# Optimization experiments

Hardware: AMD Instinct MI355X
Metric: run time of the kernel (lower is better)

Reference implementation:

```python
import jax, jax.numpy as jnp
import numpy as np

N = 50000   # nodes
E = 800000  # edges (avg degree 16)
R = 3       # relations (distance bins)
IN = 3      # node_input_dim
H = 64      # hidden_dim
EA = 6      # edge_input_dim
DH = 32     # decoder_hidden_dim


def setup_inputs() -> dict:
    key = jax.random.key(0)
    ks = jax.random.split(key, 16)
    x = jax.random.normal(ks[0], (N, IN), jnp.float32)
    edge_index = jax.random.randint(ks[1], (2, E), 0, N)
    edge_attr = jax.random.uniform(ks[2], (E, EA), dtype=jnp.float32)
    # scale log1p-distance column so edges span all 3 bins (thresholds ~8.52, ~9.21)
    edge_attr = edge_attr.at[:, 0].mul(12.0)
    p = lambda k, s: jax.random.normal(k, s, jnp.float32) * 0.1
    return dict(
        x=x, edge_index=edge_index, edge_attr=edge_attr,
        w0=p(ks[3], (R, IN, H)), root0=p(ks[4], (IN, H)), b0=jnp.zeros((H,), jnp.float32),
        w1=p(ks[5], (R, H, H)),  root1=p(ks[6], (H, H)),  b1=jnp.zeros((H,), jnp.float32),
        w2=p(ks[7], (R, H, H)),  root2=p(ks[8], (H, H)),  b2=jnp.zeros((H,), jnp.float32),
        ln_g0=jnp.ones((H,), jnp.float32), ln_b0=jnp.zeros((H,), jnp.float32),
        ln_g1=jnp.ones((H,), jnp.float32), ln_b1=jnp.zeros((H,), jnp.float32),
        ln_g2=jnp.ones((H,), jnp.float32), ln_b2=jnp.zeros((H,), jnp.float32),
        res_w=p(ks[9], (IN, H)), res_b=jnp.zeros((H,), jnp.float32),
        dec_w1=p(ks[10], (4 * H + EA, DH)), dec_b1=jnp.zeros((DH,), jnp.float32),
        dec_w2=p(ks[11], (DH, DH // 2)),    dec_b2=jnp.zeros((DH // 2,), jnp.float32),
        dec_w3=p(ks[12], (DH // 2, 1)),     dec_b3=jnp.zeros((1,), jnp.float32),
    )


def _layernorm(v, g, b, eps=1e-5):
    mu = v.mean(-1, keepdims=True)
    var = ((v - mu) ** 2).mean(-1, keepdims=True)
    return (v - mu) / jnp.sqrt(var + eps) * g + b


def reference(x, edge_index, edge_attr,
              w0, root0, b0, w1, root1, b1, w2, root2, b2,
              ln_g0, ln_b0, ln_g1, ln_b1, ln_g2, ln_b2,
              res_w, res_b,
              dec_w1, dec_b1, dec_w2, dec_b2, dec_w3, dec_b3):
    dist = edge_attr[:, 0]
    q1 = jnp.log1p(jnp.float32(5000.0))
    q2 = jnp.log1p(jnp.float32(10000.0))
    edge_type = (dist > q1).astype(jnp.int32) + (dist > q2).astype(jnp.int32)  # [E]
    src, dst = edge_index[0], edge_index[1]

    def rgcn(xi, W, root, b):
        # RGCNConv with per-relation mean aggregation:
        # out_i = root x_i + b + sum_r W_r * mean_{j in N_r(i)} x_j
        # aggregate-then-transform: segment-sum masked source feats, divide by
        # per-relation in-degree, then one small [in,H] matmul per relation.
        xs = xi[src]                                  # [E, in] gather
        out = xi @ root + b                           # [N, H]
        for r in range(R):
            m = (edge_type == r).astype(xi.dtype)[:, None]
            s = jax.ops.segment_sum(xs * m, dst, num_segments=N)   # [N, in]
            c = jax.ops.segment_sum(m, dst, num_segments=N)        # [N, 1]
            out = out + (s / jnp.maximum(c, 1.0)) @ W[r]
        return out

    # encoder (eval mode -> dropout is identity)
    h = jax.nn.relu(rgcn(x, w0, root0, b0))
    h1 = _layernorm(h + x @ res_w + res_b, ln_g0, ln_b0)
    h = jax.nn.relu(rgcn(h1, w1, root1, b1))
    h2 = _layernorm(h + h1, ln_g1, ln_b1)
    h = jax.nn.relu(rgcn(h2, w2, root2, b2))
    h3 = _layernorm(h + h2, ln_g2, ln_b2)

    # edge decoder
    hs, hd = h3[src], h3[dst]                         # [E, H] gathers
    dec_in = jnp.concatenate([hs, hd, jnp.abs(hs - hd), hs * hd, edge_attr], axis=-1)
    z = jax.nn.relu(dec_in @ dec_w1 + dec_b1)
    z = jax.nn.relu(z @ dec_w2 + dec_b2)
    return (z @ dec_w3 + dec_b3).squeeze(-1)          # [E]
```

## Files before the change

kernel.cpp:

```cpp
#include <hip/hip_runtime.h>
#include <math.h>

#define NN 50000
#define NE 800000
#define HD 64
#define NB 196
#define DT 5

typedef float f32x4 __attribute__((ext_vector_type(4)));
typedef float f32x16 __attribute__((ext_vector_type(16)));
typedef short short8 __attribute__((ext_vector_type(8)));
typedef _Float16 hf2 __attribute__((ext_vector_type(2)));
typedef _Float16 half8 __attribute__((ext_vector_type(8)));

__device__ __forceinline__ float wave_sum(float v) {
  #pragma unroll
  for (int off = 32; off > 0; off >>= 1) v += __shfl_xor(v, off, 64);
  return v;
}

__device__ __forceinline__ unsigned f2h_pk(float a, float b) {
  auto v = __builtin_amdgcn_cvt_pkrtz(a, b);
  union { decltype(v) h; unsigned u; } cv; cv.h = v; return cv.u;
}
__device__ __forceinline__ unsigned short f2h(float a) {
  union { _Float16 h; unsigned short u; } cv; cv.h = (_Float16)a; return cv.u;
}
__device__ __forceinline__ float h2f(unsigned short b) {
  union { unsigned short u; _Float16 h; } v; v.u = b; return (float)v.h;
}

__global__ __launch_bounds__(256) void edge_prep(
    const int* __restrict__ ei, const float* __restrict__ ea,
    int* __restrict__ cntR, unsigned char* __restrict__ r8)
{
  int e = blockIdx.x * blockDim.x + threadIdx.x;
  if (e >= NE) return;
  float dist = ea[e * 6];
  const float q1 = log1pf(5000.0f);
  const float q2 = log1pf(10000.0f);
  int r = (dist > q1 ? 1 : 0) + (dist > q2 ? 1 : 0);
  r8[e] = (unsigned char)r;
  int d = ei[NE + e];
  atomicAdd(&cntR[d * 3 + r], 1);
}

__global__ __launch_bounds__(256) void scanA(const int* __restrict__ cntR, int* __restrict__ bsum) {
  __shared__ int sd[256];
  int n = blockIdx.x * 256 + threadIdx.x;
  int deg = 0;
  if (n < NN) deg = cntR[3 * n] + cntR[3 * n + 1] + cntR[3 * n + 2];
  sd[threadIdx.x] = deg;
  __syncthreads();
  #pragma unroll
  for (int s = 128; s > 0; s >>= 1) {
    if (threadIdx.x < s) sd[threadIdx.x] += sd[threadIdx.x + s];
    __syncthreads();
  }
  if (threadIdx.x == 0) bsum[blockIdx.x] = sd[0];
}

__global__ __launch_bounds__(256) void scanB(int* __restrict__ bsum) {
  __shared__ int sd[256];
  int v = (threadIdx.x < NB) ? bsum[threadIdx.x] : 0;
  sd[threadIdx.x] = v;
  __syncthreads();
  for (int s = 1; s < 256; s <<= 1) {
    int t = (threadIdx.x >= s) ? sd[threadIdx.x - s] : 0;
    __syncthreads();
    sd[threadIdx.x] += t;
    __syncthreads();
  }
  if (threadIdx.x < NB) bsum[threadIdx.x] = sd[threadIdx.x] - v;
}

__global__ __launch_bounds__(256) void scanC(
    const int* __restrict__ cntR, const int* __restrict__ bsum,
    int* __restrict__ off3, int* __restrict__ cursor3, float* __restrict__ dinv)
{
  __shared__ int sd[256];
  int n = blockIdx.x * 256 + threadIdx.x;
  int c0 = 0, c1 = 0, c2 = 0;
  if (n < NN) { c0 = cntR[3 * n]; c1 = cntR[3 * n + 1]; c2 = cntR[3 * n + 2]; }
  int deg = c0 + c1 + c2;
  sd[threadIdx.x] = deg;
  __syncthreads();
  for (int s = 1; s < 256; s <<= 1) {
    int t = (threadIdx.x >= s) ? sd[threadIdx.x - s] : 0;
    __syncthreads();
    sd[threadIdx.x] += t;
    __syncthreads();
  }
  if (n < NN) {
    int o = bsum[blockIdx.x] + sd[threadIdx.x] - deg;
    off3[3 * n + 0] = o;           cursor3[3 * n + 0] = o;
    off3[3 * n + 1] = o + c0;      cursor3[3 * n + 1] = o + c0;
    off3[3 * n + 2] = o + c0 + c1; cursor3[3 * n + 2] = o + c0 + c1;
    dinv[3 * n + 0] = 1.0f / (float)(c0 > 1 ? c0 : 1);
    dinv[3 * n + 1] = 1.0f / (float)(c1 > 1 ? c1 : 1);
    dinv[3 * n + 2] = 1.0f / (float)(c2 > 1 ? c2 : 1);
  }
}

__global__ __launch_bounds__(256) void scatter_kernel(
    const int* __restrict__ ei, const unsigned char* __restrict__ r8,
    int* __restrict__ cursor3, unsigned short* __restrict__ sorted)
{
  int e = blockIdx.x * blockDim.x + threadIdx.x;
  if (e >= NE) return;
  int r = r8[e];
  int s = ei[e], d = ei[NE + e];
  int pos = atomicAdd(&cursor3[d * 3 + r], 1);
  sorted[pos] = (unsigned short)s;
}

__global__ __launch_bounds__(256) void agg0_pack(
    const float* __restrict__ x, const int* __restrict__ off3, const int* __restrict__ cntR,
    const unsigned short* __restrict__ sorted, float* __restrict__ agg0,
    const float* __restrict__ W1, const float* __restrict__ W2,
    const float* __restrict__ root1, const float* __restrict__ w1,
    const float* __restrict__ root2, const float* __restrict__ w2,
    unsigned short* __restrict__ pk3, unsigned short* __restrict__ pk2,
    unsigned short* __restrict__ pkl1, unsigned short* __restrict__ pkl2)
{
  if (blockIdx.x < 3) {
    if (blockIdx.x == 0) {
      for (int idx = threadIdx.x; idx < 8704; idx += 256) {
        int j = idx & 7, l = (idx >> 3) & 63, t = idx >> 9;
        int k = 16 * t + 8 * (l >> 5) + j;
        int n = l & 31;
        pk3[idx] = (k < 262) ? f2h(W1[k * 32 + n]) : (unsigned short)0;
      }
      for (int idx = threadIdx.x; idx < 512; idx += 256) {
        int j = idx & 7, l = idx >> 3;
        int k = (l >> 4) * 8 + j, n = l & 15;
        pk2[idx] = f2h(W2[k * 16 + n]);
      }
    } else {
      const float* root = (blockIdx.x == 1) ? root1 : root2;
      const float* W    = (blockIdx.x == 1) ? w1 : w2;
      unsigned short* pkL = (blockIdx.x == 1) ? pkl1 : pkl2;
      for (int idx = threadIdx.x; idx < 16384; idx += 256) {
        int j = idx & 7, l = (idx >> 3) & 63, nt = (idx >> 9) & 3, t = idx >> 11;
        int k = t * 32 + (l >> 4) * 8 + j;
        int n = nt * 16 + (l & 15);
        float w = (k < 64) ? root[k * 64 + n]
                           : W[((k - 64) >> 6) * 4096 + (k & 63) * 64 + n];
        pkL[idx] = f2h(w);
      }
    }
    return;
  }
  int wid = ((blockIdx.x - 3) * blockDim.x + threadIdx.x) >> 6;
  int lane = threadIdx.x & 63;
  int n = wid * 16 + (lane >> 2);
  int f = lane & 3;
  if (n >= NN) return;
  #pragma unroll
  for (int r = 0; r < 3; r++) {
    int st = off3[3 * n + r], len = cntR[3 * n + r];
    float a = 0.f;
    int i = 0;
    for (; i + 4 <= len; i += 4) {
      int s0 = sorted[st + i], s1 = sorted[st + i + 1];
      int s2 = sorted[st + i + 2], s3 = sorted[st + i + 3];
      float v0 = (f < 3) ? x[s0 * 3 + f] : 0.f;
      float v1 = (f < 3) ? x[s1 * 3 + f] : 0.f;
      float v2 = (f < 3) ? x[s2 * 3 + f] : 0.f;
      float v3 = (f < 3) ? x[s3 * 3 + f] : 0.f;
      a += (v0 + v1) + (v2 + v3);
    }
    for (; i < len; i++) {
      int s0 = sorted[st + i];
      a += (f < 3) ? x[s0 * 3 + f] : 0.f;
    }
    if (f < 3) agg0[n * 9 + r * 3 + f] = a;
  }
}

__global__ __launch_bounds__(256) void node0_kernel(
    const float* __restrict__ x, const float* __restrict__ agg0, const float* __restrict__ dinv,
    const float* __restrict__ w0, const float* __restrict__ root0, const float* __restrict__ b0,
    const float* __restrict__ res_w, const float* __restrict__ res_b,
    const float* __restrict__ g, const float* __restrict__ bb,
    unsigned short* __restrict__ hb)
{
  int wid = __builtin_amdgcn_readfirstlane((int)((blockIdx.x * blockDim.x + threadIdx.x) >> 6));
  int lane = threadIdx.x & 63;
  int n0 = wid * 8;
  if (n0 >= NN) return;
  float wr[3], ww[9], wres[3];
  #pragma unroll
  for (int i = 0; i < 3; i++) { wr[i] = root0[i * HD + lane]; wres[i] = res_w[i * HD + lane]; }
  #pragma unroll
  for (int i = 0; i < 9; i++) ww[i] = w0[i * HD + lane];
  float vb = b0[lane], vrb = res_b[lane], vg = g[lane], vbb = bb[lane];
  #pragma unroll
  for (int k = 0; k < 8; k++) {
    int nk = n0 + k;
    float xv[3];
    #pragma unroll
    for (int i = 0; i < 3; i++) xv[i] = x[nk * 3 + i];
    float v = vb;
    #pragma unroll
    for (int i = 0; i < 3; i++) v = fmaf(xv[i], wr[i], v);
    #pragma unroll
    for (int r = 0; r < 3; r++) {
      float s = 0.f;
      #pragma unroll
      for (int i = 0; i < 3; i++) s = fmaf(agg0[nk * 9 + r * 3 + i], ww[r * 3 + i], s);
      v = fmaf(dinv[nk * 3 + r], s, v);
    }
    v = fmaxf(v, 0.f);
    float res = vrb;
    #pragma unroll
    for (int i = 0; i < 3; i++) res = fmaf(xv[i], wres[i], res);
    float t = v + res;
    float mu = wave_sum(t) * 0.015625f;
    float dt = t - mu;
    float var = wave_sum(dt * dt) * 0.015625f;
    float o = dt * rsqrtf(var + 1e-5f) * vg + vbb;
    hb[(size_t)nk * HD + lane] = f2h(o);
  }
}

__global__ __launch_bounds__(256) void layer_fused(
    const unsigned short* __restrict__ hb_in, const unsigned short* __restrict__ pkL,
    const float* __restrict__ bias, const float* __restrict__ g, const float* __restrict__ bb,
    const int* __restrict__ off3, const int* __restrict__ cntR,
    const unsigned short* __restrict__ sorted, const float* __restrict__ dinv,
    unsigned short* __restrict__ hb_out)
{
  __shared__ unsigned short tile[4][16][256];
  int wv = threadIdx.x >> 6;
  int lane = threadIdx.x & 63;
  int wid = (blockIdx.x * blockDim.x + threadIdx.x) >> 6;
  int n0 = wid * 16;
  if (n0 >= NN) return;
  char* T = (char*)&tile[wv][0][0];

  {
    int m = lane >> 2;
    int q = lane & 3;
    int node = n0 + m;
    int swz = (m & 7) << 4;
    const unsigned short* hrow = hb_in + (size_t)node * HD + q * 16;
    uint4 rv0 = *(const uint4*)(hrow);
    uint4 rv1 = *(const uint4*)(hrow + 8);
    *(uint4*)(T + m * 512 + ((q * 32) ^ swz))      = rv0;
    *(uint4*)(T + m * 512 + ((q * 32 + 16) ^ swz)) = rv1;

    union U4 { uint4 u; hf2 h[4]; };
    #pragma unroll
    for (int r = 0; r < 3; r++) {
      int st = off3[node * 3 + r];
      int len = cntR[node * 3 + r];
      hf2 acc[8];
      #pragma unroll
      for (int j = 0; j < 8; j++) acc[j] = (hf2){(_Float16)0.f, (_Float16)0.f};
      int i = 0;
      for (; i + 4 <= len; i += 4) {
        int s0 = sorted[st + i],     s1 = sorted[st + i + 1];
        int s2 = sorted[st + i + 2], s3 = sorted[st + i + 3];
        const uint4* p0 = (const uint4*)(hb_in + (size_t)s0 * HD + q * 16);
        const uint4* p1 = (const uint4*)(hb_in + (size_t)s1 * HD + q * 16);
        const uint4* p2 = (const uint4*)(hb_in + (size_t)s2 * HD + q * 16);
        const uint4* p3 = (const uint4*)(hb_in + (size_t)s3 * HD + q * 16);
        U4 a0, a1, b0, b1, c0, c1, d0, d1;
        a0.u = p0[0]; a1.u = p0[1];
        b0.u = p1[0]; b1.u = p1[1];
        c0.u = p2[0]; c1.u = p2[1];
        d0.u = p3[0]; d1.u = p3[1];
        #pragma unroll
        for (int k = 0; k < 4; k++) {
          acc[k]     += (a0.h[k] + b0.h[k]) + (c0.h[k] + d0.h[k]);
          acc[4 + k] += (a1.h[k] + b1.h[k]) + (c1.h[k] + d1.h[k]);
        }
      }
      for (; i < len; i++) {
        int s0 = sorted[st + i];
        const uint4* p0 = (const uint4*)(hb_in + (size_t)s0 * HD + q * 16);
        U4 u0, u1;
        u0.u = p0[0]; u1.u = p0[1];
        #pragma unroll
        for (int k = 0; k < 4; k++) {
          acc[k]     += u0.h[k];
          acc[4 + k] += u1.h[k];
        }
      }
      float dv = dinv[node * 3 + r];
      unsigned pk[8];
      #pragma unroll
      for (int j = 0; j < 8; j++)
        pk[j] = f2h_pk((float)acc[j][0] * dv, (float)acc[j][1] * dv);
      uint4 w0 = make_uint4(pk[0], pk[1], pk[2], pk[3]);
      uint4 w1 = make_uint4(pk[4], pk[5], pk[6], pk[7]);
      *(uint4*)(T + m * 512 + ((128 + r * 128 + q * 32) ^ swz))      = w0;
      *(uint4*)(T + m * 512 + ((128 + r * 128 + q * 32 + 16) ^ swz)) = w1;
    }
  }

  asm volatile("s_waitcnt lgkmcnt(0)" ::: "memory");
  __builtin_amdgcn_sched_barrier(0);

  int m2 = lane & 15, gq = lane >> 4;
  int swz2 = (m2 & 7) << 4;
  const half8* Bp = (const half8*)pkL;
  f32x4 acc[4];
  #pragma unroll
  for (int nt = 0; nt < 4; nt++) acc[nt] = (f32x4){0.f, 0.f, 0.f, 0.f};
  #pragma unroll
  for (int t = 0; t < 8; t++) {
    union AF { short8 s; half8 h; } af;
    af.s = *(const short8*)(T + m2 * 512 + ((gq * 16 + t * 64) ^ swz2));
    #pragma unroll
    for (int nt = 0; nt < 4; nt++)
      acc[nt] = __builtin_amdgcn_mfma_f32_16x16x32_f16(af.h, Bp[(t * 4 + nt) * 64 + lane], acc[nt], 0, 0, 0);
  }

  float bias_v[4], g_v[4], bb_v[4];
  #pragma unroll
  for (int nt = 0; nt < 4; nt++) {
    bias_v[nt] = bias[nt * 16 + m2];
    g_v[nt] = g[nt * 16 + m2];
    bb_v[nt] = bb[nt * 16 + m2];
  }
  #pragma unroll
  for (int rr = 0; rr < 4; rr++) {
    int lrow = gq * 4 + rr;
    int nodeo = n0 + lrow;
    int swzr = (lrow & 7) << 4;
    float tv[4], s = 0.f;
    #pragma unroll
    for (int nt = 0; nt < 4; nt++) {
      unsigned short rh = *(const unsigned short*)(T + lrow * 512 + (((nt * 16 + m2) * 2) ^ swzr));
      float res = h2f(rh);
      float v = fmaxf(acc[nt][rr] + bias_v[nt], 0.f) + res;
      tv[nt] = v; s += v;
    }
    #pragma unroll
    for (int o = 1; o < 16; o <<= 1) s += __shfl_xor(s, o, 64);
    float mu = s * 0.015625f;
    float s2 = 0.f;
    #pragma unroll
    for (int nt = 0; nt < 4; nt++) { float dd = tv[nt] - mu; s2 += dd * dd; }
    #pragma unroll
    for (int o = 1; o < 16; o <<= 1) s2 += __shfl_xor(s2, o, 64);
    float rstd = rsqrtf(s2 * 0.015625f + 1e-5f);
    #pragma unroll
    for (int nt = 0; nt < 4; nt++) {
      float o = (tv[nt] - mu) * rstd * g_v[nt] + bb_v[nt];
      hb_out[(size_t)nodeo * HD + nt * 16 + m2] = f2h(o);
    }
  }
}

__global__ __launch_bounds__(256) void decoder_mfma(
    const unsigned short* __restrict__ hb, const int* __restrict__ ei, const float* __restrict__ ea,
    const unsigned short* __restrict__ pk3, const unsigned short* __restrict__ pk2,
    const float* __restrict__ B1, const float* __restrict__ B2,
    const float* __restrict__ W3, const float* __restrict__ B3,
    float* __restrict__ out)
{
  __shared__ float Zl[4 * 32 * 33];
  __shared__ unsigned short Bsh[8704 + 512];
  {
    unsigned* dsh = (unsigned*)Bsh;
    const unsigned* sp3 = (const unsigned*)pk3;
    for (int i = threadIdx.x; i < 4352; i += 256) dsh[i] = sp3[i];
    const unsigned* sp2 = (const unsigned*)pk2;
    if (threadIdx.x < 256) dsh[4352 + threadIdx.x] = sp2[threadIdx.x];
  }
  __syncthreads();

  int wv = threadIdx.x >> 6;
  int lane = threadIdx.x & 63;
  int r = lane & 31, u = lane >> 5;
  int base = (blockIdx.x * 4 + wv) * 32 * DT;

  int m = lane & 15, g = lane >> 4;
  float b1v = B1[r];
  float bias2 = B2[m];
  float w3v = W3[m];
  float b3v = B3[0];
  float* Z = Zl + wv * 1056;
  const half8* Bp  = (const half8*)Bsh;
  const half8* Bp2 = (const half8*)(Bsh + 8704);

  union u8h { short8 s8; half8 h8; hf2 h[4]; unsigned w[4]; };

  u8h hsA[4], hdA[4], hsB[4], hdB[4];
  float2 E0[3], E1[3], E2[3];

  auto GATH = [&](u8h* Hs, u8h* Hd, int s, int d) {
    const unsigned short* ps = hb + (size_t)s * HD + u * 8;
    const unsigned short* pq = hb + (size_t)d * HD + u * 8;
    #pragma unroll
    for (int t = 0; t < 4; t++) {
      Hs[t].s8 = *(const short8*)(ps + t * 16);
      Hd[t].s8 = *(const short8*)(pq + t * 16);
    }
  };
  auto LDEA = [&](float2* E, int e0t) {
    if (u == 0) {
      const float* er = ea + (size_t)(e0t + r) * 6;
      E[0] = *(const float2*)(er);
      E[1] = *(const float2*)(er + 2);
      E[2] = *(const float2*)(er + 4);
    }
  };
  auto COMP = [&](u8h* Hs, u8h* Hd, float2* E, int e0t) {
    u8h ad[4], pd[4];
    #pragma unroll
    for (int t = 0; t < 4; t++) {
      #pragma unroll
      for (int k = 0; k < 4; k++) {
        union { hf2 h; unsigned u; } dd;
        dd.h = Hs[t].h[k] - Hd[t].h[k];
        ad[t].w[k] = dd.u & 0x7FFF7FFFu;
        pd[t].h[k] = Hs[t].h[k] * Hd[t].h[k];
      }
    }
    u8h aea;
    aea.w[0] = 0; aea.w[1] = 0; aea.w[2] = 0; aea.w[3] = 0;
    if (u == 0) {
      aea.w[0] = f2h_pk(E[0].x, E[0].y);
      aea.w[1] = f2h_pk(E[1].x, E[1].y);
      aea.w[2] = f2h_pk(E[2].x, E[2].y);
    }

    f32x16 acc = {0.f, 0.f, 0.f, 0.f, 0.f, 0.f, 0.f, 0.f,
                  0.f, 0.f, 0.f, 0.f, 0.f, 0.f, 0.f, 0.f};
    #pragma unroll
    for (int t = 0; t < 4; t++)
      acc = __builtin_amdgcn_mfma_f32_32x32x16_f16(Hs[t].h8, Bp[t * 64 + lane], acc, 0, 0, 0);
    #pragma unroll
    for (int t = 0; t < 4; t++)
      acc = __builtin_amdgcn_mfma_f32_32x32x16_f16(Hd[t].h8, Bp[(4 + t) * 64 + lane], acc, 0, 0, 0);
    #pragma unroll
    for (int t = 0; t < 4; t++)
      acc = __builtin_amdgcn_mfma_f32_32x32x16_f16(ad[t].h8, Bp[(8 + t) * 64 + lane], acc, 0, 0, 0);
    #pragma unroll
    for (int t = 0; t < 4; t++)
      acc = __builtin_amdgcn_mfma_f32_32x32x16_f16(pd[t].h8, Bp[(12 + t) * 64 + lane], acc, 0, 0, 0);
    acc = __builtin_amdgcn_mfma_f32_32x32x16_f16(aea.h8, Bp[16 * 64 + lane], acc, 0, 0, 0);

    #pragma unroll
    for (int i = 0; i < 16; i++) {
      int row = (i & 3) + 8 * (i >> 2) + 4 * u;
      Z[r * 33 + row] = fmaxf(acc[i] + b1v, 0.f);
    }

    #pragma unroll
    for (int q = 0; q < 2; q++) {
      u8h A2;
      #pragma unroll
      for (int j2 = 0; j2 < 4; j2++)
        A2.w[j2] = f2h_pk(Z[(g * 8 + 2 * j2) * 33 + q * 16 + m],
                          Z[(g * 8 + 2 * j2 + 1) * 33 + q * 16 + m]);
      f32x4 acc2 = {0.f, 0.f, 0.f, 0.f};
      acc2 = __builtin_amdgcn_mfma_f32_16x16x32_f16(A2.h8, Bp2[lane], acc2, 0, 0, 0);

      float t0 = fmaxf(acc2[0] + bias2, 0.f) * w3v;
      float t1 = fmaxf(acc2[1] + bias2, 0.f) * w3v;
      float t2 = fmaxf(acc2[2] + bias2, 0.f) * w3v;
      float t3 = fmaxf(acc2[3] + bias2, 0.f) * w3v;
      #pragma unroll
      for (int off = 1; off < 16; off <<= 1) {
        t0 += __shfl_xor(t0, off, 64);
        t1 += __shfl_xor(t1, off, 64);
        t2 += __shfl_xor(t2, off, 64);
        t3 += __shfl_xor(t3, off, 64);
      }
      if (m < 4) {
        float val = (m == 0) ? t0 : (m == 1) ? t1 : (m == 2) ? t2 : t3;
        out[e0t + q * 16 + g * 4 + m] = val + b3v;
      }
    }
  };

  int s1, d1;
  {
    int s0 = ei[base + r], d0 = ei[NE + base + r];
    LDEA(E0, base);
    GATH(hsA, hdA, s0, d0);
  }
  s1 = ei[base + 32 + r]; d1 = ei[NE + base + 32 + r];
  LDEA(E1, base + 32);

  #pragma unroll
  for (int t = 0; t < DT; t++) {
    if (t + 1 < DT) GATH(hsB, hdB, s1, d1);
    int s2 = 0, d2 = 0;
    if (t + 2 < DT) {
      s2 = ei[base + (t + 2) * 32 + r]; d2 = ei[NE + base + (t + 2) * 32 + r];
      LDEA(E2, base + (t + 2) * 32);
    }
    COMP(hsA, hdA, E0, base + t * 32);
    #pragma unroll
    for (int k = 0; k < 4; k++) { hsA[k] = hsB[k]; hdA[k] = hdB[k]; }
    E0[0] = E1[0]; E0[1] = E1[1]; E0[2] = E1[2];
    E1[0] = E2[0]; E1[1] = E2[1]; E1[2] = E2[2];
    s1 = s2; d1 = d2;
  }
}

extern "C" void kernel_launch(void* const* d_in, const int* in_sizes, int n_in,
                              void* d_out, int out_size, void* d_ws, size_t ws_size,
                              hipStream_t stream) {
  const float* x      = (const float*)d_in[0];
  const int*   ei     = (const int*)d_in[1];
  const float* ea     = (const float*)d_in[2];
  const float* w0     = (const float*)d_in[3];
  const float* root0  = (const float*)d_in[4];
  const float* b0     = (const float*)d_in[5];
  const float* w1     = (const float*)d_in[6];
  const float* root1  = (const float*)d_in[7];
  const float* b1     = (const float*)d_in[8];
  const float* w2     = (const float*)d_in[9];
  const float* root2  = (const float*)d_in[10];
  const float* b2     = (const float*)d_in[11];
  const float* ln_g0  = (const float*)d_in[12];
  const float* ln_b0  = (const float*)d_in[13];
  const float* ln_g1  = (const float*)d_in[14];
  const float* ln_b1  = (const float*)d_in[15];
  const float* ln_g2  = (const float*)d_in[16];
  const float* ln_b2  = (const float*)d_in[17];
  const float* res_w  = (const float*)d_in[18];
  const float* res_b  = (const float*)d_in[19];
  const float* dec_w1 = (const float*)d_in[20];
  const float* dec_b1 = (const float*)d_in[21];
  const float* dec_w2 = (const float*)d_in[22];
  const float* dec_b2 = (const float*)d_in[23];
  const float* dec_w3 = (const float*)d_in[24];
  const float* dec_b3 = (const float*)d_in[25];

  char* ws = (char*)d_ws;
  unsigned char* r8 = (unsigned char*)(ws + 0);
  int*   cntR    = (int*)(ws + 800000);
  float* agg0    = (float*)(ws + 1400000);
  int*   bsum    = (int*)(ws + 3200000);
  int*   off3    = (int*)(ws + 3201024);
  int*   cursor3 = (int*)(ws + 3801024);
  float* dinv    = (float*)(ws + 4401024);
  unsigned short* sorted = (unsigned short*)(ws + 5001024);
  unsigned short* pk3  = (unsigned short*)(ws + 6601024);
  unsigned short* pkw2 = (unsigned short*)(ws + 6618432);
  unsigned short* pkl1 = (unsigned short*)(ws + 6619456);
  unsigned short* pkl2 = (unsigned short*)(ws + 6652224);
  unsigned short* hb   = (unsigned short*)(ws + 6684992);
  unsigned short* hb2  = (unsigned short*)(ws + 13084992);

  hipMemsetAsync(cntR, 0, 600000, stream);

  edge_prep<<<(NE + 255) / 256, 256, 0, stream>>>(ei, ea, cntR, r8);
  scanA<<<NB, 256, 0, stream>>>(cntR, bsum);
  scanB<<<1, 256, 0, stream>>>(bsum);
  scanC<<<NB, 256, 0, stream>>>(cntR, bsum, off3, cursor3, dinv);
  scatter_kernel<<<(NE + 255) / 256, 256, 0, stream>>>(ei, r8, cursor3, sorted);
  agg0_pack<<<3 + (NN + 63) / 64, 256, 0, stream>>>(x, off3, cntR, sorted, agg0,
                                                    dec_w1, dec_w2, root1, w1, root2, w2,
                                                    pk3, pkw2, pkl1, pkl2);

  const int node0_blocks = (NN / 8 + 3) / 4;
  const int fused_blocks = (NN / 16 + 3) / 4;

  node0_kernel<<<node0_blocks, 256, 0, stream>>>(x, agg0, dinv, w0, root0, b0,
                                                 res_w, res_b, ln_g0, ln_b0, hb);

  layer_fused<<<fused_blocks, 256, 0, stream>>>(hb, pkl1, b1, ln_g1, ln_b1,
                                                off3, cntR, sorted, dinv, hb2);
  layer_fused<<<fused_blocks, 256, 0, stream>>>(hb2, pkl2, b2, ln_g2, ln_b2,
                                                off3, cntR, sorted, dinv, hb);

  decoder_mfma<<<NE / (128 * DT), 256, 0, stream>>>(hb, ei, ea, pk3, pkw2, dec_b1,
                                                    dec_b2, dec_w3, dec_b3, (float*)d_out);
}
```

Measured before the change: 326.1 us.

## Replace global-atomic CSR build with two-level bucketed sort using shared-memory atomics

Replaces the per-edge global atomic histogram and scatter with a two-level scheme. Edges are first bucketed by destination high byte into packed 32-bit records, using block-local histograms and one global atomic per bucket. Per-bucket kernels then compute the per-(node, relation) counts and place source indices using shared-memory cursors. This cuts contended global atomics and makes the final scatter writes more local, at the cost of extra kernel launches and an intermediate 3.2 MB record buffer pass.

```diff
diff --git a/kernel.cpp b/kernel.cpp
--- a/kernel.cpp
+++ b/kernel.cpp
@@ -5,6 +5,8 @@
 #define NE 800000
 #define HD 64
 #define NB 196
+#define NBK 196
+#define BSE 2048
 #define DT 5
 
 typedef float f32x4 __attribute__((ext_vector_type(4)));
@@ -30,19 +32,123 @@
   union { unsigned short u; _Float16 h; } v; v.u = b; return (float)v.h;
 }
 
-__global__ __launch_bounds__(256) void edge_prep(
+__global__ __launch_bounds__(256) void bucket_count(
+    const int* __restrict__ ei, int* __restrict__ bcnt)
+{
+  __shared__ int h[NBK];
+  for (int i = threadIdx.x; i < NBK; i += 256) h[i] = 0;
+  __syncthreads();
+  int e0 = blockIdx.x * BSE;
+  #pragma unroll
+  for (int k = 0; k < BSE / 256; k++) {
+    int e = e0 + k * 256 + threadIdx.x;
+    if (e < NE) atomicAdd(&h[ei[NE + e] >> 8], 1);
+  }
+  __syncthreads();
+  for (int i = threadIdx.x; i < NBK; i += 256)
+    if (h[i]) atomicAdd(&bcnt[i], h[i]);
+}
+
+__global__ __launch_bounds__(256) void bucket_scan(
+    const int* __restrict__ bcnt, int* __restrict__ bbase, int* __restrict__ bcur)
+{
+  __shared__ int sd[256];
+  int v = (threadIdx.x < NBK) ? bcnt[threadIdx.x] : 0;
+  sd[threadIdx.x] = v;
+  __syncthreads();
+  for (int s = 1; s < 256; s <<= 1) {
+    int t = (threadIdx.x >= s) ? sd[threadIdx.x - s] : 0;
+    __syncthreads();
+    sd[threadIdx.x] += t;
+    __syncthreads();
+  }
+  if (threadIdx.x < NBK) {
+    int ex = sd[threadIdx.x] - v;
+    bbase[threadIdx.x] = ex;
+    bcur[threadIdx.x] = ex;
+  }
+  if (threadIdx.x == 0) bbase[NBK] = NE;
+}
+
+__global__ __launch_bounds__(256) void bucket_scatter(
     const int* __restrict__ ei, const float* __restrict__ ea,
-    int* __restrict__ cntR, unsigned char* __restrict__ r8)
-{
-  int e = blockIdx.x * blockDim.x + threadIdx.x;
-  if (e >= NE) return;
-  float dist = ea[e * 6];
+    int* __restrict__ bcur, unsigned* __restrict__ recs)
+{
+  __shared__ int hcnt[NBK], hbase[NBK];
+  for (int i = threadIdx.x; i < NBK; i += 256) hcnt[i] = 0;
+  __syncthreads();
   const float q1 = log1pf(5000.0f);
   const float q2 = log1pf(10000.0f);
-  int r = (dist > q1 ? 1 : 0) + (dist > q2 ? 1 : 0);
-  r8[e] = (unsigned char)r;
-  int d = ei[NE + e];
-  atomicAdd(&cntR[d * 3 + r], 1);
+  int e0 = blockIdx.x * BSE;
+  unsigned rec[BSE / 256];
+  int bk[BSE / 256];
+  #pragma unroll
+  for (int k = 0; k < BSE / 256; k++) {
+    int e = e0 + k * 256 + threadIdx.x;
+    bk[k] = -1;
+    if (e < NE) {
+      int s = ei[e], d = ei[NE + e];
+      float dist = ea[(size_t)e * 6];
+      int r = (dist > q1 ? 1 : 0) + (dist > q2 ? 1 : 0);
+      rec[k] = (unsigned)s | ((unsigned)(d & 255) << 16) | ((unsigned)r << 24);
+      bk[k] = d >> 8;
+      atomicAdd(&hcnt[bk[k]], 1);
+    }
+  }
+  __syncthreads();
+  for (int i = threadIdx.x; i < NBK; i += 256) {
+    hbase[i] = hcnt[i] ? atomicAdd(&bcur[i], hcnt[i]) : 0;
+    hcnt[i] = 0;
+  }
+  __syncthreads();
+  #pragma unroll
+  for (int k = 0; k < BSE / 256; k++) {
+    if (bk[k] >= 0) {
+      int idx = atomicAdd(&hcnt[bk[k]], 1);
+      recs[hbase[bk[k]] + idx] = rec[k];
+    }
+  }
+}
+
+__global__ __launch_bounds__(256) void bucket_hist(
+    const unsigned* __restrict__ recs, const int* __restrict__ bbase,
+    int* __restrict__ cntR)
+{
+  __shared__ int h[768];
+  for (int i = threadIdx.x; i < 768; i += 256) h[i] = 0;
+  __syncthreads();
+  int b = blockIdx.x;
+  int lo = bbase[b], hi = bbase[b + 1];
+  for (int i = lo + threadIdx.x; i < hi; i += 256) {
+    unsigned rec = recs[i];
+    int dlow = (rec >> 16) & 255, r = (rec >> 24) & 3;
+    atomicAdd(&h[dlow * 3 + r], 1);
+  }
+  __syncthreads();
+  for (int i = threadIdx.x; i < 768; i += 256) {
+    int n = b * 256 + i / 3;
+    if (n < NN) cntR[n * 3 + i % 3] = h[i];
+  }
+}
+
+__global__ __launch_bounds__(256) void bucket_place(
+    const unsigned* __restrict__ recs, const int* __restrict__ bbase,
+    const int* __restrict__ off3, unsigned short* __restrict__ sorted)
+{
+  __shared__ int cur[768];
+  int b = blockIdx.x;
+  for (int i = threadIdx.x; i < 768; i += 256) {
+    int n = b * 256 + i / 3;
+    cur[i] = (n < NN) ? off3[n * 3 + i % 3] : 0;
+  }
+  __syncthreads();
+  int lo = bbase[b], hi = bbase[b + 1];
+  for (int i = lo + threadIdx.x; i < hi; i += 256) {
+    unsigned rec = recs[i];
+    int s = rec & 0xFFFF, dlow = (rec >> 16) & 255, r = (rec >> 24) & 3;
+    int pos = atomicAdd(&cur[dlow * 3 + r], 1);
+    sorted[pos] = (unsigned short)s;
+  }
 }
 
 __global__ __launch_bounds__(256) void scanA(const int* __restrict__ cntR, int* __restrict__ bsum) {
@@ -76,7 +182,7 @@
 
 __global__ __launch_bounds__(256) void scanC(
     const int* __restrict__ cntR, const int* __restrict__ bsum,
-    int* __restrict__ off3, int* __restrict__ cursor3, float* __restrict__ dinv)
+    int* __restrict__ off3, float* __restrict__ dinv)
 {
   __shared__ int sd[256];
   int n = blockIdx.x * 256 + threadIdx.x;
@@ -93,25 +199,13 @@
   }
   if (n < NN) {
     int o = bsum[blockIdx.x] + sd[threadIdx.x] - deg;
-    off3[3 * n + 0] = o;           cursor3[3 * n + 0] = o;
-    off3[3 * n + 1] = o + c0;      cursor3[3 * n + 1] = o + c0;
-    off3[3 * n + 2] = o + c0 + c1; cursor3[3 * n + 2] = o + c0 + c1;
+    off3[3 * n + 0] = o;
+    off3[3 * n + 1] = o + c0;
+    off3[3 * n + 2] = o + c0 + c1;
     dinv[3 * n + 0] = 1.0f / (float)(c0 > 1 ? c0 : 1);
     dinv[3 * n + 1] = 1.0f / (float)(c1 > 1 ? c1 : 1);
     dinv[3 * n + 2] = 1.0f / (float)(c2 > 1 ? c2 : 1);
   }
-}
-
-__global__ __launch_bounds__(256) void scatter_kernel(
-    const int* __restrict__ ei, const unsigned char* __restrict__ r8,
-    int* __restrict__ cursor3, unsigned short* __restrict__ sorted)
-{
-  int e = blockIdx.x * blockDim.x + threadIdx.x;
-  if (e >= NE) return;
-  int r = r8[e];
-  int s = ei[e], d = ei[NE + e];
-  int pos = atomicAdd(&cursor3[d * 3 + r], 1);
-  sorted[pos] = (unsigned short)s;
 }
 
 __global__ __launch_bounds__(256) void agg0_pack(
@@ -536,28 +630,36 @@
   const float* dec_b3 = (const float*)d_in[25];
 
   char* ws = (char*)d_ws;
-  unsigned char* r8 = (unsigned char*)(ws + 0);
-  int*   cntR    = (int*)(ws + 800000);
-  float* agg0    = (float*)(ws + 1400000);
-  int*   bsum    = (int*)(ws + 3200000);
-  int*   off3    = (int*)(ws + 3201024);
-  int*   cursor3 = (int*)(ws + 3801024);
-  float* dinv    = (float*)(ws + 4401024);
-  unsigned short* sorted = (unsigned short*)(ws + 5001024);
-  unsigned short* pk3  = (unsigned short*)(ws + 6601024);
-  unsigned short* pkw2 = (unsigned short*)(ws + 6618432);
-  unsigned short* pkl1 = (unsigned short*)(ws + 6619456);
-  unsigned short* pkl2 = (unsigned short*)(ws + 6652224);
-  unsigned short* hb   = (unsigned short*)(ws + 6684992);
-  unsigned short* hb2  = (unsigned short*)(ws + 13084992);
-
-  hipMemsetAsync(cntR, 0, 600000, stream);
-
-  edge_prep<<<(NE + 255) / 256, 256, 0, stream>>>(ei, ea, cntR, r8);
+  unsigned* recs = (unsigned*)(ws + 0);
+  int*   bcnt    = (int*)(ws + 3200000);
+  int*   bbase   = (int*)(ws + 3201024);
+  int*   bcur    = (int*)(ws + 3202048);
+  float* agg0    = (float*)(ws + 3203072);
+  int*   bsum    = (int*)(ws + 5003072);
+  int*   off3    = (int*)(ws + 5004096);
+  float* dinv    = (float*)(ws + 5604096);
+  int*   cntR    = (int*)(ws + 6204096);
+  unsigned short* sorted = (unsigned short*)(ws + 6804096);
+  unsigned short* pk3  = (unsigned short*)(ws + 8404096);
+  unsigned short* pkw2 = (unsigned short*)(ws + 8421504);
+  unsigned short* pkl1 = (unsigned short*)(ws + 8422528);
+  unsigned short* pkl2 = (unsigned short*)(ws + 8455296);
+  unsigned short* hb   = (unsigned short*)(ws + 8488064);
+  unsigned short* hb2  = (unsigned short*)(ws + 14888064);
+
+  hipMemsetAsync(bcnt, 0, 1024, stream);
+
+  const int sort_blocks = (NE + BSE - 1) / BSE;
+
+  bucket_count<<<sort_blocks, 256, 0, stream>>>(ei, bcnt);
+  bucket_scan<<<1, 256, 0, stream>>>(bcnt, bbase, bcur);
+  bucket_scatter<<<sort_blocks, 256, 0, stream>>>(ei, ea, bcur, recs);
+  bucket_hist<<<NBK, 256, 0, stream>>>(recs, bbase, cntR);
   scanA<<<NB, 256, 0, stream>>>(cntR, bsum);
   scanB<<<1, 256, 0, stream>>>(bsum);
-  scanC<<<NB, 256, 0, stream>>>(cntR, bsum, off3, cursor3, dinv);
-  scatter_kernel<<<(NE + 255) / 256, 256, 0, stream>>>(ei, r8, cursor3, sorted);
+  scanC<<<NB, 256, 0, stream>>>(cntR, bsum, off3, dinv);
+  bucket_place<<<NBK, 256, 0, stream>>>(recs, bbase, off3, sorted);
+
   agg0_pack<<<3 + (NN + 63) / 64, 256, 0, stream>>>(x, off3, cntR, sorted, agg0,
                                                     dec_w1, dec_w2, root1, w1, root2, w2,
                                                     pk3, pkw2, pkl1, pkl2);
```

Result: faster. 273.8 us (-16.0%).
